# Optimization experiments

Measured on AMD Instinct MI355X. Metric: run time of the kernel, lower is better.

The kernel has to match this reference:

```python
import math
import jax, jax.numpy as jnp
import numpy as np

B, T, C, H = 2, 2048, 1024, 16

def setup_inputs() -> dict:
    key = jax.random.key(0)
    k1, k2, k3 = jax.random.split(key, 3)
    x = jax.random.normal(k1, (B, T, C), dtype=jnp.float32)
    W_kqv = jax.random.normal(k2, (C, 3 * C), dtype=jnp.float32) * (1.0 / math.sqrt(C))
    W_proj = jax.random.normal(k3, (C, C), dtype=jnp.float32) * (1.0 / math.sqrt(C))
    b_proj = jnp.zeros((C,), dtype=jnp.float32)
    return {"x": x, "W_kqv": W_kqv, "W_proj": W_proj, "b_proj": b_proj}

def reference(x, W_kqv, W_proj, b_proj):
    Bx, Tx, Cx = x.shape
    hs = Cx // H  # head size
    q, k, v = jnp.split(x @ W_kqv, 3, axis=2)  # each (B,T,C)
    # (B,T,C) -> (B,H,T,hs)
    q = q.reshape(Bx, Tx, H, hs).transpose(0, 2, 1, 3)
    k = k.reshape(Bx, Tx, H, hs).transpose(0, 2, 1, 3)
    v = v.reshape(Bx, Tx, H, hs).transpose(0, 2, 1, 3)
    attn = jnp.einsum('bhqd,bhkd->bhqk', q, k) / math.sqrt(hs)  # (B,H,T,T)
    causal = jnp.tril(jnp.ones((Tx, Tx), dtype=bool))
    attn = jnp.where(causal, attn, -jnp.inf)
    attn = jax.nn.softmax(attn, axis=-1)
    y = jnp.einsum('bhqk,bhkd->bhqd', attn, v)  # (B,H,T,hs)
    y = y.transpose(0, 2, 1, 3).reshape(Bx, Tx, Cx)
    return y @ W_proj + b_proj
```

## Files before the change

### kernel.cpp

```cpp
#include <hip/hip_runtime.h>


typedef unsigned short u16;
typedef unsigned int u32;
typedef __bf16 bf16x8 __attribute__((ext_vector_type(8)));
typedef float f32x4 __attribute__((ext_vector_type(4)));
typedef u32 u32x4 __attribute__((ext_vector_type(4)));
typedef u16 u16x4 __attribute__((ext_vector_type(4)));

__device__ __forceinline__ u16 f2bf(float f) {
  u32 u = __float_as_uint(f);
  u32 r = u + 0x7FFFu + ((u >> 16) & 1u);
  return (u16)(r >> 16);
}

__device__ __forceinline__ bf16x8 ld_bf8(const u16* p) {
  union { u32x4 u; bf16x8 b; } x;
  x.u = *(const u32x4*)p;
  return x.b;
}

__device__ __forceinline__ void gld_lds16(const u16* g, u16* l) {
  __builtin_amdgcn_global_load_lds(
      (const __attribute__((address_space(1))) u32*)g,
      (__attribute__((address_space(3))) u32*)l, 16, 0, 0);
}

__device__ __forceinline__ void convT_body(const float* __restrict__ src,
                                           u16* __restrict__ dst, int R, int Cc,
                                           int r0, int c0, float* ls ) {
  int t = threadIdx.x;
  for (int u = t; u < 1024; u += 256) {
    int r = u >> 4, cs = (u & 15) << 2;
    float4 v = *(const float4*)&src[(size_t)(r0 + r) * Cc + (c0 + cs)];
    ls[r * 65 + cs] = v.x; ls[r * 65 + cs + 1] = v.y;
    ls[r * 65 + cs + 2] = v.z; ls[r * 65 + cs + 3] = v.w;
  }
  __syncthreads();
  for (int u = t; u < 1024; u += 256) {
    int n = u >> 4, ks = (u & 15) << 2;
    u16x4 o;
    o.x = f2bf(ls[ks * 65 + n]); o.y = f2bf(ls[(ks + 1) * 65 + n]);
    o.z = f2bf(ls[(ks + 2) * 65 + n]); o.w = f2bf(ls[(ks + 3) * 65 + n]);
    *(u16x4*)&dst[(size_t)(c0 + n) * R + (r0 + ks)] = o;
  }
}

__global__ __launch_bounds__(256) void prep_kernel(
    const float* __restrict__ x, const float* __restrict__ Wkqv,
    const float* __restrict__ Wproj, u16* __restrict__ xb,
    u16* __restrict__ wkqvT, u16* __restrict__ wprojT) {
  __shared__ float ls[64 * 65];
  int bx = blockIdx.x;
  if (bx < 2048) {
    int idx = bx * 256 + threadIdx.x;
    const float4* s4 = (const float4*)x;
    float4 a = s4[2 * idx], b = s4[2 * idx + 1];
    union { u16 h[8]; u32x4 v; } pk;
    pk.h[0] = f2bf(a.x); pk.h[1] = f2bf(a.y); pk.h[2] = f2bf(a.z); pk.h[3] = f2bf(a.w);
    pk.h[4] = f2bf(b.x); pk.h[5] = f2bf(b.y); pk.h[6] = f2bf(b.z); pk.h[7] = f2bf(b.w);
    *(u32x4*)&xb[(size_t)idx * 8] = pk.v;
  } else if (bx < 2816) {
    int idx = bx - 2048;
    convT_body(Wkqv, wkqvT, 1024, 3072, (idx & 15) * 64, (idx >> 4) * 64, ls);
  } else {
    int idx = bx - 2816;
    convT_body(Wproj, wprojT, 1024, 1024, (idx & 15) * 64, (idx >> 4) * 64, ls);
  }
}

__global__ __launch_bounds__(256) void qkv_gemm_kernel(
    const u16* __restrict__ A, const u16* __restrict__ Bt,
    u16* __restrict__ Qh, u16* __restrict__ Kh, u16* __restrict__ Vh, float qscale) {
  constexpr int K = 1024;
  __shared__ __align__(16) u16 As[128 * 32];
  __shared__ __align__(16) u16 Bs[128 * 32];
  int t = threadIdx.x;
  int wave = t >> 6, lane = t & 63, quad = lane >> 4, l16 = lane & 15;
  int wm = (wave >> 1) << 6, wn = (wave & 1) << 6;
  int m0 = blockIdx.x * 128, n0 = blockIdx.y * 128;
  f32x4 acc[4][4] = {};
  int u0 = t, u1 = t + 256;
  int ra0 = u0 >> 2, ca0 = ((u0 & 3) ^ ((u0 >> 3) & 3)) << 3;
  int ra1 = u1 >> 2, ca1 = ((u1 & 3) ^ ((u1 >> 3) & 3)) << 3;
  int swq = (quad ^ ((l16 >> 1) & 3)) << 3;
  for (int k0 = 0; k0 < K; k0 += 32) {
    gld_lds16(&A[(size_t)(m0 + ra0) * K + k0 + ca0], &As[u0 * 8]);
    gld_lds16(&A[(size_t)(m0 + ra1) * K + k0 + ca1], &As[u1 * 8]);
    gld_lds16(&Bt[(size_t)(n0 + ra0) * K + k0 + ca0], &Bs[u0 * 8]);
    gld_lds16(&Bt[(size_t)(n0 + ra1) * K + k0 + ca1], &Bs[u1 * 8]);
    __syncthreads();
    bf16x8 af[4], bfr[4];
    for (int r = 0; r < 4; ++r) af[r] = ld_bf8(&As[(wm + r * 16 + l16) * 32 + swq]);
    for (int c = 0; c < 4; ++c) bfr[c] = ld_bf8(&Bs[(wn + c * 16 + l16) * 32 + swq]);
    for (int r = 0; r < 4; ++r)
      for (int c = 0; c < 4; ++c)
        acc[r][c] = __builtin_amdgcn_mfma_f32_16x16x32_bf16(af[r], bfr[c], acc[r][c], 0, 0, 0);
    __syncthreads();
  }
  for (int r = 0; r < 4; ++r) {
    int rowbase = m0 + wm + r * 16 + quad * 4;
    for (int c = 0; c < 4; ++c) {
      int col = n0 + wn + c * 16 + l16;
      int seg = col >> 10;
      int cc = col & 1023;
      int h = cc >> 6, d = cc & 63;
      for (int i = 0; i < 4; ++i) {
        int row = rowbase + i;
        int b = row >> 11, tt = row & 2047;
        size_t off = (((size_t)(b * 16 + h)) * 2048 + tt) * 64 + d;
        float v = acc[r][c][i];
        if (seg == 0)      Qh[off] = f2bf(v * qscale);
        else if (seg == 1) Kh[off] = f2bf(v);
        else               Vh[off] = f2bf(v);
      }
    }
  }
}

__global__ __launch_bounds__(256) void vT_kernel(const u16* __restrict__ Vh,
                                                 u16* __restrict__ Vt) {
  __shared__ __align__(16) u16 ls[64 * 72];
  int t = threadIdx.x;
  int t0 = blockIdx.x * 64, bh = blockIdx.y;
  const u16* in = Vh + ((size_t)bh * 2048 + t0) * 64;
  for (int u = t; u < 512; u += 256) {
    int row = u >> 3, col = (u & 7) << 3;
    *(u32x4*)&ls[row * 72 + col] = *(const u32x4*)&in[(size_t)row * 64 + col];
  }
  __syncthreads();
  for (int u = t; u < 512; u += 256) {
    int d = u >> 3, tc = (u & 7) << 3;
    union { u16 h[8]; u32x4 v; } pk;
    for (int j = 0; j < 8; ++j) pk.h[j] = ls[(tc + j) * 72 + d];
    *(u32x4*)&Vt[((size_t)bh * 64 + d) * 2048 + t0 + tc] = pk.v;
  }
}

__global__ __launch_bounds__(256) void proj_gemm_kernel(
    const u16* __restrict__ A, const u16* __restrict__ Bt,
    float* __restrict__ out, const float* __restrict__ bias) {
  constexpr int K = 1024;
  __shared__ __align__(16) u16 As[64 * 32];
  __shared__ __align__(16) u16 Bs[64 * 32];
  int t = threadIdx.x;
  int wave = t >> 6, lane = t & 63, quad = lane >> 4, l16 = lane & 15;
  int wm = (wave >> 1) << 5, wn = (wave & 1) << 5;
  int m0 = blockIdx.x * 64, n0 = blockIdx.y * 64;
  f32x4 acc[2][2] = {};
  int u0 = t;
  int ra0 = u0 >> 2, ca0 = ((u0 & 3) ^ ((u0 >> 3) & 3)) << 3;
  int swq = (quad ^ ((l16 >> 1) & 3)) << 3;
  for (int k0 = 0; k0 < K; k0 += 32) {
    gld_lds16(&A[(size_t)(m0 + ra0) * K + k0 + ca0], &As[u0 * 8]);
    gld_lds16(&Bt[(size_t)(n0 + ra0) * K + k0 + ca0], &Bs[u0 * 8]);
    __syncthreads();
    bf16x8 af[2], bfr[2];
    for (int r = 0; r < 2; ++r) af[r] = ld_bf8(&As[(wm + r * 16 + l16) * 32 + swq]);
    for (int c = 0; c < 2; ++c) bfr[c] = ld_bf8(&Bs[(wn + c * 16 + l16) * 32 + swq]);
    for (int r = 0; r < 2; ++r)
      for (int c = 0; c < 2; ++c)
        acc[r][c] = __builtin_amdgcn_mfma_f32_16x16x32_bf16(af[r], bfr[c], acc[r][c], 0, 0, 0);
    __syncthreads();
  }
  for (int r = 0; r < 2; ++r) {
    int rowbase = m0 + wm + r * 16 + quad * 4;
    for (int c = 0; c < 2; ++c) {
      int col = n0 + wn + c * 16 + l16;
      float bv = bias[col];
      for (int i = 0; i < 4; ++i)
        out[(size_t)(rowbase + i) * 1024 + col] = acc[r][c][i] + bv;
    }
  }
}

__global__ __launch_bounds__(256, 6) void flash_kernel(
    const u16* __restrict__ Qh, const u16* __restrict__ Kh, const u16* __restrict__ Vt,
    u16* __restrict__ yb, float* __restrict__ Opart) {
  __shared__ __align__(16) u16 Ks[64 * 64];
  __shared__ __align__(16) u16 Vs[64 * 64];
  __shared__ __align__(16) u16 Ps[64 * 64];
  int t = threadIdx.x, wave = t >> 6, lane = t & 63, quad = lane >> 4, l16 = lane & 15;
  int id = blockIdx.x;
  int g = id / 360, r = id % 360;
  int bh = g * 8 + (r & 7);
  int jx = r >> 3;
  int qtile, kvs, kve, sidx = 0, half = 0;
  bool partial;
  if (jx < 19) {
    qtile = 18 - jx; kvs = 0; kve = qtile + 1; partial = false;
  } else {
    sidx = (jx - 19) >> 1; half = (jx - 19) & 1;
    qtile = 31 - sidx;
    int nkv = qtile + 1, mid = nkv >> 1;
    kvs = half ? mid : 0; kve = half ? nkv : mid; partial = true;
  }
  int q0 = qtile << 6;
  const u16* Qb = Qh + (size_t)bh * 2048 * 64;
  const u16* Kb = Kh + (size_t)bh * 2048 * 64;
  const u16* Vb = Vt + (size_t)bh * 64 * 2048;
  bf16x8 qa0, qa1;
  {
    int qrow = q0 + wave * 16 + l16;
    qa0 = ld_bf8(&Qb[(size_t)qrow * 64 + quad * 8]);
    qa1 = ld_bf8(&Qb[(size_t)qrow * 64 + 32 + quad * 8]);
  }
  f32x4 oacc[4] = {};
  float lsum = 0.f;
  int u0 = wave * 128 + lane, u1 = u0 + 64;
  int r0 = u0 >> 3, p0 = u0 & 7, cb0 = (p0 - r0) & 7;
  int r1s = u1 >> 3, p1 = u1 & 7, cb1 = (p1 - r1s) & 7;
  for (int j = kvs; j < kve; ++j) {
    int kv0 = j << 6;
    __syncthreads();
    gld_lds16(&Kb[(size_t)(kv0 + r0) * 64 + cb0 * 8], &Ks[u0 * 8]);
    gld_lds16(&Kb[(size_t)(kv0 + r1s) * 64 + cb1 * 8], &Ks[u1 * 8]);
    gld_lds16(&Vb[(size_t)r0 * 2048 + kv0 + cb0 * 8], &Vs[u0 * 8]);
    gld_lds16(&Vb[(size_t)r1s * 2048 + kv0 + cb1 * 8], &Vs[u1 * 8]);
    __syncthreads();
    bool maskit = (j == qtile);
    for (int c = 0; c < 4; ++c) {
      int krow = c * 16 + l16;
      bf16x8 kb0 = ld_bf8(&Ks[krow * 64 + ((quad + krow) & 7) * 8]);
      bf16x8 kb1 = ld_bf8(&Ks[krow * 64 + ((quad + 4 + krow) & 7) * 8]);
      f32x4 z = {0.f, 0.f, 0.f, 0.f};
      z = __builtin_amdgcn_mfma_f32_16x16x32_bf16(kb0, qa0, z, 0, 0, 0);
      z = __builtin_amdgcn_mfma_f32_16x16x32_bf16(kb1, qa1, z, 0, 0, 0);
      int prow = wave * 16 + l16;
      union { u16 hh[4]; u16x4 v; } pk;
      if (maskit) {
        int qg = q0 + prow;
        for (int i = 0; i < 4; ++i) {
          float p = __builtin_amdgcn_exp2f(z[i]);
          if (kv0 + c * 16 + quad * 4 + i > qg) p = 0.f;
          lsum += p;
          pk.hh[i] = f2bf(p);
        }
      } else {
        for (int i = 0; i < 4; ++i) {
          float p = __builtin_amdgcn_exp2f(z[i]);
          lsum += p;
          pk.hh[i] = f2bf(p);
        }
      }
      *(u16x4*)&Ps[prow * 64 + ((2 * c + (quad >> 1) + prow) & 7) * 8 + (quad & 1) * 4] = pk.v;
    }
    int prow = wave * 16 + l16;
    bf16x8 pa0 = ld_bf8(&Ps[prow * 64 + ((quad + prow) & 7) * 8]);
    bf16x8 pa1 = ld_bf8(&Ps[prow * 64 + ((quad + 4 + prow) & 7) * 8]);
    for (int dt = 0; dt < 4; ++dt) {
      int vrow = dt * 16 + l16;
      bf16x8 vb0 = ld_bf8(&Vs[vrow * 64 + ((quad + vrow) & 7) * 8]);
      bf16x8 vb1 = ld_bf8(&Vs[vrow * 64 + ((quad + 4 + vrow) & 7) * 8]);
      oacc[dt] = __builtin_amdgcn_mfma_f32_16x16x32_bf16(pa0, vb0, oacc[dt], 0, 0, 0);
      oacc[dt] = __builtin_amdgcn_mfma_f32_16x16x32_bf16(pa1, vb1, oacc[dt], 0, 0, 0);
    }
  }
  lsum += __shfl_xor(lsum, 16);
  lsum += __shfl_xor(lsum, 32);
  if (partial) {
    float* Op = Opart + ((size_t)(bh * 13 + sidx) * 2 + half) * 4160;
    for (int dt = 0; dt < 4; ++dt)
      for (int i = 0; i < 4; ++i)
        Op[(wave * 16 + quad * 4 + i) * 64 + dt * 16 + l16] = oacc[dt][i];
    if (quad == 0) Op[4096 + wave * 16 + l16] = lsum;
  } else {
    int b = bh >> 4, h = bh & 15;
    for (int i = 0; i < 4; ++i) {
      float inv = 1.0f / __shfl(lsum, quad * 4 + i);
      int qq = q0 + wave * 16 + quad * 4 + i;
      size_t rowoff = ((size_t)(b * 2048 + qq)) * 1024 + h * 64;
      for (int dt = 0; dt < 4; ++dt)
        yb[rowoff + dt * 16 + l16] = f2bf(oacc[dt][i] * inv);
    }
  }
}

__global__ __launch_bounds__(256) void combine_kernel(const float* __restrict__ Opart,
                                                      u16* __restrict__ yb) {
  int sidx = blockIdx.x, bh = blockIdx.y, t = threadIdx.x;
  int qtile = 31 - sidx;
  const float* A = Opart + (size_t)(bh * 13 + sidx) * 2 * 4160;
  const float* Bp = A + 4160;
  int q = t >> 2, d0 = (t & 3) << 4;
  float inv = 1.0f / (A[4096 + q] + Bp[4096 + q]);
  int b = bh >> 4, h = bh & 15;
  size_t off = ((size_t)(b * 2048 + (qtile << 6) + q)) * 1024 + h * 64 + d0;
  union { u16 hh[16]; u32x4 v[2]; } pk;
  for (int k = 0; k < 16; ++k)
    pk.hh[k] = f2bf((A[q * 64 + d0 + k] + Bp[q * 64 + d0 + k]) * inv);
  *(u32x4*)&yb[off] = pk.v[0];
  *(u32x4*)&yb[off + 8] = pk.v[1];
}

extern "C" void kernel_launch(void* const* d_in, const int* in_sizes, int n_in,
                              void* d_out, int out_size, void* d_ws, size_t ws_size,
                              hipStream_t stream) {
  const float* x     = (const float*)d_in[0];
  const float* Wkqv  = (const float*)d_in[1];
  const float* Wproj = (const float*)d_in[2];
  const float* bproj = (const float*)d_in[3];
  float* out = (float*)d_out;

  u16* ws     = (u16*)d_ws;
  u16* xb     = ws;
  u16* wkqvT  = xb + (size_t)4096 * 1024;
  u16* wprojT = wkqvT + (size_t)3072 * 1024;
  u16* Qh     = wprojT + (size_t)1024 * 1024;
  u16* Kh     = Qh + (size_t)32 * 2048 * 64;
  u16* Vt     = Kh + (size_t)32 * 2048 * 64;
  u16* yb     = Vt + (size_t)32 * 2048 * 64;
  u16* Vh     = yb;
  float* Opart = (float*)ws;

  const float QSCALE = 0.18033688011112042f;

  prep_kernel<<<3072, 256, 0, stream>>>(x, Wkqv, Wproj, xb, wkqvT, wprojT);
  qkv_gemm_kernel<<<dim3(32, 24), 256, 0, stream>>>(xb, wkqvT, Qh, Kh, Vh, QSCALE);
  vT_kernel<<<dim3(32, 32), 256, 0, stream>>>(Vh, Vt);
  flash_kernel<<<1440, 256, 0, stream>>>(Qh, Kh, Vt, yb, Opart);
  combine_kernel<<<dim3(13, 32), 256, 0, stream>>>(Opart, yb);
  proj_gemm_kernel<<<dim3(64, 16), 256, 0, stream>>>(yb, wprojT, out, bproj);
}
```

Baseline: 179.7 us.

## Double-buffer K/V tiles in flash attention and raise MFMA wave priority

The flash attention loop now keeps two LDS buffers for K and V. The next tile's global-to-LDS loads are issued right after a single barrier, so they overlap with the current tile's QK^T, softmax and PV work, replacing the two barriers per iteration. MFMA sections are wrapped in s_setprio to favour waves that are issuing matrix ops. The extra LDS (and the launch bound dropping from 6 to 4 blocks per CU) lowers occupancy, which may offset the overlap gain.

```diff
diff --git a/kernel.cpp b/kernel.cpp
--- a/kernel.cpp
+++ b/kernel.cpp
@@ -174,11 +174,11 @@
   }
 }
 
-__global__ __launch_bounds__(256, 6) void flash_kernel(
+__global__ __launch_bounds__(256, 4) void flash_kernel(
     const u16* __restrict__ Qh, const u16* __restrict__ Kh, const u16* __restrict__ Vt,
     u16* __restrict__ yb, float* __restrict__ Opart) {
-  __shared__ __align__(16) u16 Ks[64 * 64];
-  __shared__ __align__(16) u16 Vs[64 * 64];
+  __shared__ __align__(16) u16 Ks[2][64 * 64];
+  __shared__ __align__(16) u16 Vs[2][64 * 64];
   __shared__ __align__(16) u16 Ps[64 * 64];
   int t = threadIdx.x, wave = t >> 6, lane = t & 63, quad = lane >> 4, l16 = lane & 15;
   int id = blockIdx.x;
@@ -210,37 +210,54 @@
   int u0 = wave * 128 + lane, u1 = u0 + 64;
   int r0 = u0 >> 3, p0 = u0 & 7, cb0 = (p0 - r0) & 7;
   int r1s = u1 >> 3, p1 = u1 & 7, cb1 = (p1 - r1s) & 7;
+  {
+    int kv0 = kvs << 6;
+    gld_lds16(&Kb[(size_t)(kv0 + r0) * 64 + cb0 * 8], &Ks[0][u0 * 8]);
+    gld_lds16(&Kb[(size_t)(kv0 + r1s) * 64 + cb1 * 8], &Ks[0][u1 * 8]);
+    gld_lds16(&Vb[(size_t)r0 * 2048 + kv0 + cb0 * 8], &Vs[0][u0 * 8]);
+    gld_lds16(&Vb[(size_t)r1s * 2048 + kv0 + cb1 * 8], &Vs[0][u1 * 8]);
+  }
   for (int j = kvs; j < kve; ++j) {
+    int p = (j - kvs) & 1;
+    asm volatile("s_waitcnt vmcnt(0)" ::: "memory");
+    __builtin_amdgcn_s_barrier();
+    asm volatile("" ::: "memory");
+    if (j + 1 < kve) {
+      int kn0 = (j + 1) << 6;
+      int pn = p ^ 1;
+      gld_lds16(&Kb[(size_t)(kn0 + r0) * 64 + cb0 * 8], &Ks[pn][u0 * 8]);
+      gld_lds16(&Kb[(size_t)(kn0 + r1s) * 64 + cb1 * 8], &Ks[pn][u1 * 8]);
+      gld_lds16(&Vb[(size_t)r0 * 2048 + kn0 + cb0 * 8], &Vs[pn][u0 * 8]);
+      gld_lds16(&Vb[(size_t)r1s * 2048 + kn0 + cb1 * 8], &Vs[pn][u1 * 8]);
+    }
     int kv0 = j << 6;
-    __syncthreads();
-    gld_lds16(&Kb[(size_t)(kv0 + r0) * 64 + cb0 * 8], &Ks[u0 * 8]);
-    gld_lds16(&Kb[(size_t)(kv0 + r1s) * 64 + cb1 * 8], &Ks[u1 * 8]);
-    gld_lds16(&Vb[(size_t)r0 * 2048 + kv0 + cb0 * 8], &Vs[u0 * 8]);
-    gld_lds16(&Vb[(size_t)r1s * 2048 + kv0 + cb1 * 8], &Vs[u1 * 8]);
-    __syncthreads();
     bool maskit = (j == qtile);
+    const u16* Ksp = Ks[p];
+    const u16* Vsp = Vs[p];
     for (int c = 0; c < 4; ++c) {
       int krow = c * 16 + l16;
-      bf16x8 kb0 = ld_bf8(&Ks[krow * 64 + ((quad + krow) & 7) * 8]);
-      bf16x8 kb1 = ld_bf8(&Ks[krow * 64 + ((quad + 4 + krow) & 7) * 8]);
+      bf16x8 kb0 = ld_bf8(&Ksp[krow * 64 + ((quad + krow) & 7) * 8]);
+      bf16x8 kb1 = ld_bf8(&Ksp[krow * 64 + ((quad + 4 + krow) & 7) * 8]);
       f32x4 z = {0.f, 0.f, 0.f, 0.f};
+      __builtin_amdgcn_s_setprio(1);
       z = __builtin_amdgcn_mfma_f32_16x16x32_bf16(kb0, qa0, z, 0, 0, 0);
       z = __builtin_amdgcn_mfma_f32_16x16x32_bf16(kb1, qa1, z, 0, 0, 0);
+      __builtin_amdgcn_s_setprio(0);
       int prow = wave * 16 + l16;
       union { u16 hh[4]; u16x4 v; } pk;
       if (maskit) {
         int qg = q0 + prow;
         for (int i = 0; i < 4; ++i) {
-          float p = __builtin_amdgcn_exp2f(z[i]);
-          if (kv0 + c * 16 + quad * 4 + i > qg) p = 0.f;
-          lsum += p;
-          pk.hh[i] = f2bf(p);
+          float pexp = __builtin_amdgcn_exp2f(z[i]);
+          if (kv0 + c * 16 + quad * 4 + i > qg) pexp = 0.f;
+          lsum += pexp;
+          pk.hh[i] = f2bf(pexp);
         }
       } else {
         for (int i = 0; i < 4; ++i) {
-          float p = __builtin_amdgcn_exp2f(z[i]);
-          lsum += p;
-          pk.hh[i] = f2bf(p);
+          float pexp = __builtin_amdgcn_exp2f(z[i]);
+          lsum += pexp;
+          pk.hh[i] = f2bf(pexp);
         }
       }
       *(u16x4*)&Ps[prow * 64 + ((2 * c + (quad >> 1) + prow) & 7) * 8 + (quad & 1) * 4] = pk.v;
@@ -250,10 +267,12 @@
     bf16x8 pa1 = ld_bf8(&Ps[prow * 64 + ((quad + 4 + prow) & 7) * 8]);
     for (int dt = 0; dt < 4; ++dt) {
       int vrow = dt * 16 + l16;
-      bf16x8 vb0 = ld_bf8(&Vs[vrow * 64 + ((quad + vrow) & 7) * 8]);
-      bf16x8 vb1 = ld_bf8(&Vs[vrow * 64 + ((quad + 4 + vrow) & 7) * 8]);
+      bf16x8 vb0 = ld_bf8(&Vsp[vrow * 64 + ((quad + vrow) & 7) * 8]);
+      bf16x8 vb1 = ld_bf8(&Vsp[vrow * 64 + ((quad + 4 + vrow) & 7) * 8]);
+      __builtin_amdgcn_s_setprio(1);
       oacc[dt] = __builtin_amdgcn_mfma_f32_16x16x32_bf16(pa0, vb0, oacc[dt], 0, 0, 0);
       oacc[dt] = __builtin_amdgcn_mfma_f32_16x16x32_bf16(pa1, vb1, oacc[dt], 0, 0, 0);
+      __builtin_amdgcn_s_setprio(0);
     }
   }
   lsum += __shfl_xor(lsum, 16);
```

New measurement: 181.2 us. About the same (+0.9%).

## Keep softmax P in registers via transposed PV MFMA, drop LDS round-trip

Applied to the files above, without the earlier changes.

Removes the Ps shared buffer: the exponentiated scores are packed to bf16 with v_cvt_pk_bf16_f32 and fed directly as the MFMA B operand, with V read from LDS in 8-byte chunks to form the A operand so the output is computed transposed. This eliminates an LDS write/read of P per KV tile and frees shared memory, which may allow higher occupancy. Output stores are vectorized accordingly, and the final normalization no longer needs shuffles. The cost is more, smaller LDS reads for V and a change in rounding (hardware conversion instead of the manual rounding helper).

```diff
diff --git a/kernel.cpp b/kernel.cpp
--- a/kernel.cpp
+++ b/kernel.cpp
@@ -6,12 +6,19 @@
 typedef __bf16 bf16x8 __attribute__((ext_vector_type(8)));
 typedef float f32x4 __attribute__((ext_vector_type(4)));
 typedef u32 u32x4 __attribute__((ext_vector_type(4)));
+typedef u32 u32x2 __attribute__((ext_vector_type(2)));
 typedef u16 u16x4 __attribute__((ext_vector_type(4)));
 
 __device__ __forceinline__ u16 f2bf(float f) {
   u32 u = __float_as_uint(f);
   u32 r = u + 0x7FFFu + ((u >> 16) & 1u);
   return (u16)(r >> 16);
+}
+
+__device__ __forceinline__ u32 cvt_pk_bf16(float a, float b) {
+  u32 r;
+  asm("v_cvt_pk_bf16_f32 %0, %1, %2" : "=v"(r) : "v"(a), "v"(b));
+  return r;
 }
 
 __device__ __forceinline__ bf16x8 ld_bf8(const u16* p) {
@@ -179,7 +186,6 @@
     u16* __restrict__ yb, float* __restrict__ Opart) {
   __shared__ __align__(16) u16 Ks[64 * 64];
   __shared__ __align__(16) u16 Vs[64 * 64];
-  __shared__ __align__(16) u16 Ps[64 * 64];
   int t = threadIdx.x, wave = t >> 6, lane = t & 63, quad = lane >> 4, l16 = lane & 15;
   int id = blockIdx.x;
   int g = id / 360, r = id % 360;
@@ -210,6 +216,8 @@
   int u0 = wave * 128 + lane, u1 = u0 + 64;
   int r0 = u0 >> 3, p0 = u0 & 7, cb0 = (p0 - r0) & 7;
   int r1s = u1 >> 3, p1 = u1 & 7, cb1 = (p1 - r1s) & 7;
+  int vsub = (quad & 1) * 4;
+  int vc0 = quad >> 1;
   for (int j = kvs; j < kve; ++j) {
     int kv0 = j << 6;
     __syncthreads();
@@ -219,6 +227,7 @@
     gld_lds16(&Vb[(size_t)r1s * 2048 + kv0 + cb1 * 8], &Vs[u1 * 8]);
     __syncthreads();
     bool maskit = (j == qtile);
+    u32 w[4][2];
     for (int c = 0; c < 4; ++c) {
       int krow = c * 16 + l16;
       bf16x8 kb0 = ld_bf8(&Ks[krow * 64 + ((quad + krow) & 7) * 8]);
@@ -226,52 +235,61 @@
       f32x4 z = {0.f, 0.f, 0.f, 0.f};
       z = __builtin_amdgcn_mfma_f32_16x16x32_bf16(kb0, qa0, z, 0, 0, 0);
       z = __builtin_amdgcn_mfma_f32_16x16x32_bf16(kb1, qa1, z, 0, 0, 0);
-      int prow = wave * 16 + l16;
-      union { u16 hh[4]; u16x4 v; } pk;
+      float pexp[4];
       if (maskit) {
-        int qg = q0 + prow;
+        int qg = q0 + wave * 16 + l16;
         for (int i = 0; i < 4; ++i) {
           float p = __builtin_amdgcn_exp2f(z[i]);
           if (kv0 + c * 16 + quad * 4 + i > qg) p = 0.f;
           lsum += p;
-          pk.hh[i] = f2bf(p);
+          pexp[i] = p;
         }
       } else {
         for (int i = 0; i < 4; ++i) {
           float p = __builtin_amdgcn_exp2f(z[i]);
           lsum += p;
-          pk.hh[i] = f2bf(p);
+          pexp[i] = p;
         }
       }
-      *(u16x4*)&Ps[prow * 64 + ((2 * c + (quad >> 1) + prow) & 7) * 8 + (quad & 1) * 4] = pk.v;
-    }
-    int prow = wave * 16 + l16;
-    bf16x8 pa0 = ld_bf8(&Ps[prow * 64 + ((quad + prow) & 7) * 8]);
-    bf16x8 pa1 = ld_bf8(&Ps[prow * 64 + ((quad + 4 + prow) & 7) * 8]);
+      w[c][0] = cvt_pk_bf16(pexp[0], pexp[1]);
+      w[c][1] = cvt_pk_bf16(pexp[2], pexp[3]);
+    }
+    union { u32 uu[4]; bf16x8 b; } pf0, pf1;
+    pf0.uu[0] = w[0][0]; pf0.uu[1] = w[0][1]; pf0.uu[2] = w[1][0]; pf0.uu[3] = w[1][1];
+    pf1.uu[0] = w[2][0]; pf1.uu[1] = w[2][1]; pf1.uu[2] = w[3][0]; pf1.uu[3] = w[3][1];
     for (int dt = 0; dt < 4; ++dt) {
       int vrow = dt * 16 + l16;
-      bf16x8 vb0 = ld_bf8(&Vs[vrow * 64 + ((quad + vrow) & 7) * 8]);
-      bf16x8 vb1 = ld_bf8(&Vs[vrow * 64 + ((quad + 4 + vrow) & 7) * 8]);
-      oacc[dt] = __builtin_amdgcn_mfma_f32_16x16x32_bf16(pa0, vb0, oacc[dt], 0, 0, 0);
-      oacc[dt] = __builtin_amdgcn_mfma_f32_16x16x32_bf16(pa1, vb1, oacc[dt], 0, 0, 0);
+      int rbase = vrow * 64 + vsub;
+      union { u32x2 lo2; struct { u32 a, b; }; } h0lo, h0hi, h1lo, h1hi;
+      h0lo.lo2 = *(const u32x2*)&Vs[rbase + (((vc0)     + vrow) & 7) * 8];
+      h0hi.lo2 = *(const u32x2*)&Vs[rbase + (((vc0 + 2) + vrow) & 7) * 8];
+      h1lo.lo2 = *(const u32x2*)&Vs[rbase + (((vc0 + 4) + vrow) & 7) * 8];
+      h1hi.lo2 = *(const u32x2*)&Vs[rbase + (((vc0 + 6) + vrow) & 7) * 8];
+      union { u32 uu[4]; bf16x8 b; } va0, va1;
+      va0.uu[0] = h0lo.a; va0.uu[1] = h0lo.b; va0.uu[2] = h0hi.a; va0.uu[3] = h0hi.b;
+      va1.uu[0] = h1lo.a; va1.uu[1] = h1lo.b; va1.uu[2] = h1hi.a; va1.uu[3] = h1hi.b;
+      oacc[dt] = __builtin_amdgcn_mfma_f32_16x16x32_bf16(va0.b, pf0.b, oacc[dt], 0, 0, 0);
+      oacc[dt] = __builtin_amdgcn_mfma_f32_16x16x32_bf16(va1.b, pf1.b, oacc[dt], 0, 0, 0);
     }
   }
   lsum += __shfl_xor(lsum, 16);
   lsum += __shfl_xor(lsum, 32);
   if (partial) {
     float* Op = Opart + ((size_t)(bh * 13 + sidx) * 2 + half) * 4160;
+    int qloc = wave * 16 + l16;
     for (int dt = 0; dt < 4; ++dt)
-      for (int i = 0; i < 4; ++i)
-        Op[(wave * 16 + quad * 4 + i) * 64 + dt * 16 + l16] = oacc[dt][i];
-    if (quad == 0) Op[4096 + wave * 16 + l16] = lsum;
+      *(f32x4*)&Op[qloc * 64 + dt * 16 + quad * 4] = oacc[dt];
+    if (quad == 0) Op[4096 + qloc] = lsum;
   } else {
-    int b = bh >> 4, h = bh & 15;
-    for (int i = 0; i < 4; ++i) {
-      float inv = 1.0f / __shfl(lsum, quad * 4 + i);
-      int qq = q0 + wave * 16 + quad * 4 + i;
-      size_t rowoff = ((size_t)(b * 2048 + qq)) * 1024 + h * 64;
-      for (int dt = 0; dt < 4; ++dt)
-        yb[rowoff + dt * 16 + l16] = f2bf(oacc[dt][i] * inv);
+    int b = bh >> 4, hd = bh & 15;
+    float inv = 1.0f / lsum;
+    int qq = q0 + wave * 16 + l16;
+    size_t rowoff = ((size_t)(b * 2048 + qq)) * 1024 + hd * 64;
+    for (int dt = 0; dt < 4; ++dt) {
+      u32x2 pr;
+      pr.x = cvt_pk_bf16(oacc[dt][0] * inv, oacc[dt][1] * inv);
+      pr.y = cvt_pk_bf16(oacc[dt][2] * inv, oacc[dt][3] * inv);
+      *(u32x2*)&yb[rowoff + dt * 16 + quad * 4] = pr;
     }
   }
 }
```

Result: no change. 181.0 us (+0.7%).
